# Kernel tuning notes

Hardware: AMD Instinct MI355X
Metric: run time of the kernel (lower is better)

The kernel has to match this reference:

```python
import jax, jax.numpy as jnp
import numpy as np

B, N, BINS = 128, 1024, 64
DEG_MAX = 50.0


def setup_inputs() -> dict:
    key = jax.random.key(0)
    k_adj, k_num = jax.random.split(key)
    # binary adjacency, edge prob 0.02 -> avg degree ~20 (fits [0, DEG_MAX] bins)
    adj = (jax.random.uniform(k_adj, (B, N, N)) < 0.02).astype(jnp.float32)
    num_nodes = jax.random.randint(k_num, (B,), 1, N + 1)
    centers = jnp.linspace(0.0, DEG_MAX, BINS, dtype=jnp.float32).reshape(BINS, 1)
    spacing = DEG_MAX / (BINS - 1)
    widths = jnp.full((BINS, 1), 1.0 / spacing, dtype=jnp.float32)
    return {"adj": adj, "num_nodes": num_nodes, "bin_center": centers, "bin_width": widths}


def reference(adj, num_nodes, bin_center, bin_width):
    # adj: [B, N, N], num_nodes: [B] int, bin_center/bin_width: [BINS, 1]
    n = adj.shape[1]
    node_mask = (jnp.arange(n)[None, :] < num_nodes[:, None]).astype(adj.dtype)  # [B, N]
    # adj[i, :n_i, :n_i] as a mask product (rows and cols beyond n_i zeroed)
    adj_m = adj * node_mask[:, :, None] * node_mask[:, None, :]

    def hist(deg):
        # deg: [B, N] -> triangular-kernel soft histogram, only valid nodes counted
        score = 1.0 - jnp.abs(deg[:, None, :] - bin_center[None]) * bin_width[None]  # [B, BINS, N]
        score = jax.nn.relu(score) * node_mask[:, None, :]
        return score.sum(2)  # [B, BINS]

    in_hist = hist(adj_m.sum(2))   # degree = row sums of the n_i x n_i block (2D .sum(1))
    out_hist = hist(adj_m.sum(1))  # degree = col sums of the n_i x n_i block (2D .sum(0))
    return jnp.stack([in_hist, out_hist])  # [2, B, BINS]
```

## Files before the change

kernel.cpp:

```cpp
#include <hip/hip_runtime.h>

#define NMAX 1024
#define BB   128
#define BINS 64
#define ROWS 32

__global__ __launch_bounds__(256) void degree_kernel(
    const float* __restrict__ adj, const int* __restrict__ num_nodes,
    float* __restrict__ in_deg, float* __restrict__ out_deg)
{
    const int b     = blockIdx.x >> 5;
    const int chunk = blockIdx.x & 31;
    const int n     = num_nodes[b];
    const int row0  = chunk * ROWS;
    if (row0 >= n) return;

    const int t    = threadIdx.x;
    const int lane = t & 63;
    const int wave = t >> 6;
    const int j0   = t * 4;
    const bool act = (j0 < n);

    const float BIG = 3.0e38f;
    const float th0 = (j0 + 0 < n) ? 0.5f : BIG;
    const float th1 = (j0 + 1 < n) ? 0.5f : BIG;
    const float th2 = (j0 + 2 < n) ? 0.5f : BIG;
    const float th3 = (j0 + 3 < n) ? 0.5f : BIG;

    float c0 = 0.f, c1 = 0.f, c2 = 0.f, c3 = 0.f;

    __shared__ float rowpart[ROWS][4];

    const int rows = min(ROWS, n - row0);
    const float4* base = (const float4*)(adj + ((size_t)b * NMAX + row0) * NMAX) + t;

    #pragma unroll 4
    for (int r = 0; r < rows; ++r) {
        float4 v = make_float4(0.f, 0.f, 0.f, 0.f);
        if (act) v = base[r * (NMAX / 4)];
        const bool p0 = v.x > th0;
        const bool p1 = v.y > th1;
        const bool p2 = v.z > th2;
        const bool p3 = v.w > th3;
        c0 += p0 ? 1.f : 0.f;
        c1 += p1 ? 1.f : 0.f;
        c2 += p2 ? 1.f : 0.f;
        c3 += p3 ? 1.f : 0.f;
        const unsigned long long b0 = __ballot(p0);
        const unsigned long long b1 = __ballot(p1);
        const unsigned long long b2 = __ballot(p2);
        const unsigned long long b3 = __ballot(p3);
        const int rs = __popcll(b0) + __popcll(b1) + __popcll(b2) + __popcll(b3);
        if (lane == 0) rowpart[r][wave] = (float)rs;
    }
    __syncthreads();

    if (t < rows) {
        const float s = rowpart[t][0] + rowpart[t][1] + rowpart[t][2] + rowpart[t][3];
        in_deg[b * NMAX + row0 + t] = s;
    }

    if (act) {
        float* op = out_deg + b * NMAX + j0;
        if (c0 != 0.f) atomicAdd(op + 0, c0);
        if (c1 != 0.f) atomicAdd(op + 1, c1);
        if (c2 != 0.f) atomicAdd(op + 2, c2);
        if (c3 != 0.f) atomicAdd(op + 3, c3);
    }
}

__global__ __launch_bounds__(256) void hist_kernel(
    const float* __restrict__ deg, const int* __restrict__ num_nodes,
    const float* __restrict__ centers, const float* __restrict__ widths,
    float* __restrict__ out)
{
    const int side = blockIdx.x >> 7;
    const int b    = blockIdx.x & 127;

    __shared__ float hist[BINS];
    __shared__ float c[BINS];
    __shared__ float w[BINS];
    if (threadIdx.x < BINS) {
        hist[threadIdx.x] = 0.f;
        c[threadIdx.x] = centers[threadIdx.x];
        w[threadIdx.x] = widths[threadIdx.x];
    }
    __syncthreads();

    const int n = num_nodes[b];
    const float inv_sp = w[0];
    const float* dp = deg + ((size_t)side * BB + b) * NMAX;

    for (int i = threadIdx.x; i < n; i += 256) {
        const float d   = dp[i];
        const float pos = d * inv_sp;
        const int   k0  = (int)floorf(pos);
        #pragma unroll
        for (int kk = 0; kk < 2; ++kk) {
            const int k = k0 + kk;
            if (k >= 0 && k < BINS) {
                const float s = 1.f - fabsf(d - c[k]) * w[k];
                if (s > 0.f) atomicAdd(&hist[k], s);
            }
        }
    }
    __syncthreads();

    if (threadIdx.x < BINS)
        out[((size_t)side * BB + b) * BINS + threadIdx.x] = hist[threadIdx.x];
}

extern "C" void kernel_launch(void* const* d_in, const int* in_sizes, int n_in,
                              void* d_out, int out_size, void* d_ws, size_t ws_size,
                              hipStream_t stream) {
    const float* adj       = (const float*)d_in[0];
    const int*   num_nodes = (const int*)d_in[1];
    const float* centers   = (const float*)d_in[2];
    const float* widths    = (const float*)d_in[3];
    float* out = (float*)d_out;

    float* deg = (float*)d_ws;
    float* in_deg  = deg;
    float* out_deg = deg + (size_t)BB * NMAX;

    hipMemsetAsync(out_deg, 0, (size_t)BB * NMAX * sizeof(float), stream);

    degree_kernel<<<BB * (NMAX / ROWS), 256, 0, stream>>>(
        adj, num_nodes, in_deg, out_deg);

    hist_kernel<<<2 * BB, 256, 0, stream>>>(
        deg, num_nodes, centers, widths, out);
}
```

Baseline: 631.5 us.

## Replace column-degree atomics with per-chunk partials reduced in hist kernel

```diff
diff --git a/kernel.cpp b/kernel.cpp
--- a/kernel.cpp
+++ b/kernel.cpp
@@ -1,13 +1,15 @@
 #include <hip/hip_runtime.h>
 
-#define NMAX 1024
-#define BB   128
-#define BINS 64
-#define ROWS 32
+#define NMAX   1024
+#define BB     128
+#define BINS   64
+#define ROWS   32
+#define NCHUNK (NMAX / ROWS)
 
 __global__ __launch_bounds__(256) void degree_kernel(
     const float* __restrict__ adj, const int* __restrict__ num_nodes,
-    float* __restrict__ in_deg, float* __restrict__ out_deg)
+    float* __restrict__ in_deg,
+    float* __restrict__ colpart)
 {
     const int b     = blockIdx.x >> 5;
     const int chunk = blockIdx.x & 31;
@@ -34,7 +36,7 @@
     const int rows = min(ROWS, n - row0);
     const float4* base = (const float4*)(adj + ((size_t)b * NMAX + row0) * NMAX) + t;
 
-    #pragma unroll 4
+    #pragma unroll 8
     for (int r = 0; r < rows; ++r) {
         float4 v = make_float4(0.f, 0.f, 0.f, 0.f);
         if (act) v = base[r * (NMAX / 4)];
@@ -61,16 +63,14 @@
     }
 
     if (act) {
-        float* op = out_deg + b * NMAX + j0;
-        if (c0 != 0.f) atomicAdd(op + 0, c0);
-        if (c1 != 0.f) atomicAdd(op + 1, c1);
-        if (c2 != 0.f) atomicAdd(op + 2, c2);
-        if (c3 != 0.f) atomicAdd(op + 3, c3);
+        float4* cp = (float4*)(colpart + (((size_t)b * NCHUNK + chunk) << 10)) + t;
+        *cp = make_float4(c0, c1, c2, c3);
     }
 }
 
 __global__ __launch_bounds__(256) void hist_kernel(
-    const float* __restrict__ deg, const int* __restrict__ num_nodes,
+    const float* __restrict__ in_deg, const float* __restrict__ colpart,
+    const int* __restrict__ num_nodes,
     const float* __restrict__ centers, const float* __restrict__ widths,
     float* __restrict__ out)
 {
@@ -88,11 +88,19 @@
     __syncthreads();
 
     const int n = num_nodes[b];
+    const int nchunks = (n + ROWS - 1) / ROWS;
     const float inv_sp = w[0];
-    const float* dp = deg + ((size_t)side * BB + b) * NMAX;
 
     for (int i = threadIdx.x; i < n; i += 256) {
-        const float d   = dp[i];
+        float d;
+        if (side == 0) {
+            d = in_deg[b * NMAX + i];
+        } else {
+            d = 0.f;
+            const float* cp = colpart + ((size_t)b * NCHUNK << 10) + i;
+            for (int ch = 0; ch < nchunks; ++ch)
+                d += cp[(size_t)ch << 10];
+        }
         const float pos = d * inv_sp;
         const int   k0  = (int)floorf(pos);
         #pragma unroll
@@ -119,15 +127,11 @@
     const float* widths    = (const float*)d_in[3];
     float* out = (float*)d_out;
 
-    float* deg = (float*)d_ws;
-    float* in_deg  = deg;
-    float* out_deg = deg + (size_t)BB * NMAX;
+    float* in_deg  = (float*)d_ws;
+    float* colpart = in_deg + (size_t)BB * NMAX;
 
-    hipMemsetAsync(out_deg, 0, (size_t)BB * NMAX * sizeof(float), stream);
+    degree_kernel<<<BB * NCHUNK, 256, 0, stream>>>(adj, num_nodes, in_deg, colpart);
 
-    degree_kernel<<<BB * (NMAX / ROWS), 256, 0, stream>>>(
-        adj, num_nodes, in_deg, out_deg);
-
-    hist_kernel<<<2 * BB, 256, 0, stream>>>(
-        deg, num_nodes, centers, widths, out);
+    hist_kernel<<<2 * BB, 256, 0, stream>>>(in_deg, colpart, num_nodes,
+                                            centers, widths, out);
 }
```

New measurement: 651.3 us. 1.03x slower.
